# Kernel tuning notes

Hardware: AMD Instinct MI355X
Metric: run time of the kernel (lower is better)

## Reference

```python
import jax, jax.numpy as jnp
import numpy as np

EPS_T = 1e-4    # min ray t to count as a hit
BIG = 1e10      # sentinel for 'no hit'
NRM_EPS = 1e-12 # F.normalize eps


def _normalize(x):
    n = jnp.linalg.norm(x, axis=-1, keepdims=True)
    return x / jnp.maximum(n, NRM_EPS)


def _to_local(d, n):
    # Build orthonormal frame (s, t, n) from normal n (Duff et al. branchless),
    # then express d in that local frame: Frame.to_local.
    sign = jnp.where(n[..., 2] >= 0.0, 1.0, -1.0)
    a = -1.0 / (sign + n[..., 2])
    b = n[..., 0] * n[..., 1] * a
    s = jnp.stack([1.0 + sign * n[..., 0] ** 2 * a, sign * b, -sign * n[..., 0]], axis=-1)
    t = jnp.stack([b, sign + n[..., 1] ** 2 * a, -n[..., 1]], axis=-1)
    return jnp.stack([jnp.sum(d * s, -1), jnp.sum(d * t, -1), jnp.sum(d * n, -1)], axis=-1)


def setup_inputs() -> dict:
    key = jax.random.key(0)
    k = jax.random.split(key, 6)
    N, S, L = 524288, 128, 64
    ray_o = jax.random.normal(k[0], (N, 3), jnp.float32) * 5.0
    ray_d = jax.random.normal(k[1], (N, 3), jnp.float32)
    centers = jax.random.normal(k[2], (S, 3), jnp.float32) * 5.0
    radii = 0.5 + jax.random.uniform(k[3], (S,), jnp.float32)
    light_pos = jax.random.normal(k[4], (L, 3), jnp.float32) * 10.0
    light_idx = jax.random.randint(k[5], (N,), 0, L, jnp.int32)
    return {"ray_o": ray_o, "ray_d": ray_d, "centers": centers, "radii": radii,
            "light_pos": light_pos, "light_idx": light_idx}


def reference(ray_o, ray_d, centers, radii, light_pos, light_idx):
    # --- shapes.intersect(rays): brute-force nearest ray-sphere hit ---
    d = _normalize(ray_d)                                   # [N,3]
    od = jnp.sum(ray_o * d, -1)                             # [N]
    b = od[:, None] - jnp.einsum('nk,sk->ns', d, centers)   # [N,S]
    c = (jnp.sum(ray_o ** 2, -1)[:, None]
         - 2.0 * jnp.einsum('nk,sk->ns', ray_o, centers)
         + jnp.sum(centers ** 2, -1)[None, :]
         - radii[None, :] ** 2)                              # [N,S]
    disc = b * b - c
    t = -b - jnp.sqrt(jnp.maximum(disc, 0.0))
    valid = (disc > 0.0) & (t > EPS_T)
    t = jnp.where(valid, t, BIG)
    tmin = jnp.min(t, axis=1)                               # [N]
    sidx = jnp.argmin(t, axis=1)                            # [N]
    active = tmin < BIG                                     # [N] bool
    p = ray_o + tmin[:, None] * d                           # hit point [N,3]
    n = _normalize(p - centers[sidx])                       # surface normal [N,3]
    # --- sample_emitter_dir_wo_isect: direction to the sampled point light ---
    ds_d = light_pos[light_idx] - p                         # [N,3]
    # --- local-frame transform + normalize + where glue ---
    local = _to_local(ds_d, n)
    results = jnp.where(active[:, None], (_normalize(local) + 1.0) / 2.0,
                        jnp.zeros_like(ds_d))
    return (1.0 + results) / 2.0, active
```

## Files before the change

kernel.cpp:

```cpp
#include <hip/hip_runtime.h>
#include <math.h>

#define EPS_T 1e-4f
#define BIG 1e10f
#define NRM_EPS 1e-12f

#define PFB(R) \
  "ds_read_b128 " R ", %[lda]\n\t" \
  "v_add_u32 %[lda], 16, %[lda]\n\t"

#define SB(W, X, Y, Z, WN, GAP) \
  W \
  "v_mul_f32 v32, %[dz], " Z "\n\t" \
  "v_mul_f32 v33, %[oz], " Z "\n\t" \
  "v_fma_f32 v32, %[dy], " Y ", v32\n\t" \
  "v_fma_f32 v33, %[oy], " Y ", v33\n\t" \
  "v_fma_f32 v32, %[dx], " X ", v32\n\t" \
  "v_fma_f32 v33, %[ox], " X ", v33\n\t" \
  "v_add_f32 v34, v32, %[nod]\n\t" \
  "v_fma_f32 v35, v33, 2.0, %[noo]\n\t" \
  "v_add_f32 v35, v35, " WN "\n\t" \
  "v_fma_f32 v35, v34, v34, v35\n\t" \
  "v_sqrt_f32 v36, v35\n\t" \
  GAP \
  "v_sub_f32 v36, v34, v36\n\t" \
  "v_cmp_lt_f32 vcc, %[eps], v36\n\t" \
  "v_cmp_gt_f32 s[20:21], %[tmin], v36\n\t" \
  "s_and_b64 vcc, vcc, s[20:21]\n\t" \
  "v_cndmask_b32 %[tmin], %[tmin], v36, vcc\n\t" \
  "v_cndmask_b32 %[sidx], %[sidx], %[vj], vcc\n\t" \
  "v_add_u32 %[vj], 1, %[vj]\n\t"

#define W4 "s_waitcnt lgkmcnt(4)\n\t"

__global__ __launch_bounds__(256) void illum_kernel(
    const float* __restrict__ ray_o,
    const float* __restrict__ ray_d,
    const float* __restrict__ centers,
    const float* __restrict__ radii,
    const float* __restrict__ light_pos,
    const int*   __restrict__ light_idx,
    float* __restrict__ out,
    int N)
{
    __shared__ float4 tab[128];

    const int tid = threadIdx.x;
    if (tid < 128) {
        float cx = centers[3 * tid + 0];
        float cy = centers[3 * tid + 1];
        float cz = centers[3 * tid + 2];
        float r  = radii[tid];
        float w  = cx * cx + cy * cy + cz * cz - r * r;
        tab[tid] = make_float4(cx, cy, cz, -w);
    }
    __syncthreads();

    const int i = blockIdx.x * blockDim.x + tid;
    if (i >= N) return;

    float ox = ray_o[3 * i + 0], oy = ray_o[3 * i + 1], oz = ray_o[3 * i + 2];
    float dx = ray_d[3 * i + 0], dy = ray_d[3 * i + 1], dz = ray_d[3 * i + 2];

    float dn  = sqrtf(dx * dx + dy * dy + dz * dz);
    float din = 1.0f / fmaxf(dn, NRM_EPS);
    dx *= din; dy *= din; dz *= din;

    const float od = ox * dx + oy * dy + oz * dz;
    const float oo = ox * ox + oy * oy + oz * oz;
    const float nod = -od;
    const float noo = -oo;

    float tmin = BIG;
    int sidx = 0, vj = 0;
    unsigned lda = (unsigned)(size_t)&tab[0];

    asm volatile(
        "s_waitcnt lgkmcnt(0)\n\t"
        PFB("v[40:43]") PFB("v[44:47]") PFB("v[48:51]") PFB("v[52:55]") PFB("v[56:59]")
        ".rept 24\n\t"
        SB(W4, "v40","v41","v42","v43", PFB("v[40:43]"))
        SB(W4, "v44","v45","v46","v47", PFB("v[44:47]"))
        SB(W4, "v48","v49","v50","v51", PFB("v[48:51]"))
        SB(W4, "v52","v53","v54","v55", PFB("v[52:55]"))
        SB(W4, "v56","v57","v58","v59", PFB("v[56:59]"))
        ".endr\n\t"
        SB(W4, "v40","v41","v42","v43", PFB("v[40:43]"))
        SB(W4, "v44","v45","v46","v47", PFB("v[44:47]"))
        SB(W4, "v48","v49","v50","v51", PFB("v[48:51]"))
        SB("s_waitcnt lgkmcnt(4)\n\t", "v52","v53","v54","v55", "s_nop 1\n\t")
        SB("s_waitcnt lgkmcnt(3)\n\t", "v56","v57","v58","v59", "s_nop 1\n\t")
        SB("s_waitcnt lgkmcnt(2)\n\t", "v40","v41","v42","v43", "s_nop 1\n\t")
        SB("s_waitcnt lgkmcnt(1)\n\t", "v44","v45","v46","v47", "s_nop 1\n\t")
        SB("s_waitcnt lgkmcnt(0)\n\t", "v48","v49","v50","v51", "s_nop 1\n\t")
        : [tmin]"+v"(tmin), [sidx]"+v"(sidx), [vj]"+v"(vj), [lda]"+v"(lda)
        : [dx]"v"(dx), [dy]"v"(dy), [dz]"v"(dz),
          [ox]"v"(ox), [oy]"v"(oy), [oz]"v"(oz),
          [nod]"v"(nod), [noo]"v"(noo),
          [eps]"s"(1e-4f)
        : "v32","v33","v34","v35","v36",
          "v40","v41","v42","v43","v44","v45","v46","v47",
          "v48","v49","v50","v51","v52","v53","v54","v55",
          "v56","v57","v58","v59",
          "s20","s21","vcc","scc","memory");

    const bool active = (tmin < BIG);

    float px = fmaf(tmin, dx, ox);
    float py = fmaf(tmin, dy, oy);
    float pz = fmaf(tmin, dz, oz);

    float4 cb = tab[sidx];
    float nx = px - cb.x, ny = py - cb.y, nz = pz - cb.z;
    float nn  = sqrtf(nx * nx + ny * ny + nz * nz);
    float nin = 1.0f / fmaxf(nn, NRM_EPS);
    nx *= nin; ny *= nin; nz *= nin;

    int li = light_idx[i];
    float dsx = light_pos[3 * li + 0] - px;
    float dsy = light_pos[3 * li + 1] - py;
    float dsz = light_pos[3 * li + 2] - pz;

    float sgn = (nz >= 0.0f) ? 1.0f : -1.0f;
    float a   = -1.0f / (sgn + nz);
    float bb  = nx * ny * a;
    float sx = 1.0f + sgn * nx * nx * a, sy = sgn * bb,          sz = -sgn * nx;
    float tx = bb,                       ty = sgn + ny * ny * a, tz = -ny;

    float l0 = dsx * sx + dsy * sy + dsz * sz;
    float l1 = dsx * tx + dsy * ty + dsz * tz;
    float l2 = dsx * nx + dsy * ny + dsz * nz;
    float ln  = sqrtf(l0 * l0 + l1 * l1 + l2 * l2);
    float lin = 1.0f / fmaxf(ln, NRM_EPS);

    float r0 = active ? (l0 * lin + 1.0f) * 0.5f : 0.0f;
    float r1 = active ? (l1 * lin + 1.0f) * 0.5f : 0.0f;
    float r2 = active ? (l2 * lin + 1.0f) * 0.5f : 0.0f;

    out[3 * i + 0] = (1.0f + r0) * 0.5f;
    out[3 * i + 1] = (1.0f + r1) * 0.5f;
    out[3 * i + 2] = (1.0f + r2) * 0.5f;
    out[(size_t)3 * N + i] = active ? 1.0f : 0.0f;
}

extern "C" void kernel_launch(void* const* d_in, const int* in_sizes, int n_in,
                              void* d_out, int out_size, void* d_ws, size_t ws_size,
                              hipStream_t stream) {
    const float* ray_o     = (const float*)d_in[0];
    const float* ray_d     = (const float*)d_in[1];
    const float* centers   = (const float*)d_in[2];
    const float* radii     = (const float*)d_in[3];
    const float* light_pos = (const float*)d_in[4];
    const int*   light_idx = (const int*)d_in[5];
    float* out = (float*)d_out;

    const int N = in_sizes[0] / 3;

    const int block = 256;
    const int grid  = (N + block - 1) / block;
    illum_kernel<<<grid, block, 0, stream>>>(ray_o, ray_d, centers, radii,
                                             light_pos, light_idx, out, N);
}
```

Before: 34.88 us.

## Stream sphere table through scalar registers via s_load instead of LDS

Precomputes the sphere table (center, negated w) in a separate one-block prep kernel written to workspace. The main kernel drops the LDS table and its block barrier, and loads spheres with s_load_dwordx16 into SGPRs in double-buffered groups of four. Sphere operands then come from scalar registers shared across the wavefront, which removes per-lane ds_read traffic and VGPR pressure. The cost is a second kernel launch, a full lgkmcnt(0) wait per group that can stall the scalar pipeline, and reading the hit sphere's center from global memory afterwards.

```diff
diff --git a/kernel.cpp b/kernel.cpp
--- a/kernel.cpp
+++ b/kernel.cpp
@@ -5,24 +5,32 @@
 #define BIG 1e10f
 #define NRM_EPS 1e-12f
 
-#define PFB(R) \
-  "ds_read_b128 " R ", %[lda]\n\t" \
-  "v_add_u32 %[lda], 16, %[lda]\n\t"
+__global__ __launch_bounds__(128) void prep_kernel(
+    const float* __restrict__ centers, const float* __restrict__ radii,
+    float4* __restrict__ tb)
+{
+    int s = threadIdx.x;
+    float cx = centers[3 * s + 0];
+    float cy = centers[3 * s + 1];
+    float cz = centers[3 * s + 2];
+    float r  = radii[s];
+    float w  = cx * cx + cy * cy + cz * cz - r * r;
+    tb[s] = make_float4(cx, cy, cz, -w);
+}
 
-#define SB(W, X, Y, Z, WN, GAP) \
-  W \
-  "v_mul_f32 v32, %[dz], " Z "\n\t" \
-  "v_mul_f32 v33, %[oz], " Z "\n\t" \
-  "v_fma_f32 v32, %[dy], " Y ", v32\n\t" \
-  "v_fma_f32 v33, %[oy], " Y ", v33\n\t" \
-  "v_fma_f32 v32, %[dx], " X ", v32\n\t" \
-  "v_fma_f32 v33, %[ox], " X ", v33\n\t" \
+#define CS(CX, CY, CZ, NW) \
+  "v_mul_f32 v32, " CZ ", %[dz]\n\t" \
+  "v_mul_f32 v33, " CZ ", %[oz]\n\t" \
+  "v_fma_f32 v32, " CY ", %[dy], v32\n\t" \
+  "v_fma_f32 v33, " CY ", %[oy], v33\n\t" \
+  "v_fma_f32 v32, " CX ", %[dx], v32\n\t" \
+  "v_fma_f32 v33, " CX ", %[ox], v33\n\t" \
   "v_add_f32 v34, v32, %[nod]\n\t" \
   "v_fma_f32 v35, v33, 2.0, %[noo]\n\t" \
-  "v_add_f32 v35, v35, " WN "\n\t" \
+  "v_add_f32 v35, " NW ", v35\n\t" \
   "v_fma_f32 v35, v34, v34, v35\n\t" \
   "v_sqrt_f32 v36, v35\n\t" \
-  GAP \
+  "s_nop 1\n\t" \
   "v_sub_f32 v36, v34, v36\n\t" \
   "v_cmp_lt_f32 vcc, %[eps], v36\n\t" \
   "v_cmp_gt_f32 s[20:21], %[tmin], v36\n\t" \
@@ -31,32 +39,30 @@
   "v_cndmask_b32 %[sidx], %[sidx], %[vj], vcc\n\t" \
   "v_add_u32 %[vj], 1, %[vj]\n\t"
 
-#define W4 "s_waitcnt lgkmcnt(4)\n\t"
+#define CGA CS("s36","s37","s38","s39") CS("s40","s41","s42","s43") \
+            CS("s44","s45","s46","s47") CS("s48","s49","s50","s51")
+#define CGB CS("s52","s53","s54","s55") CS("s56","s57","s58","s59") \
+            CS("s60","s61","s62","s63") CS("s64","s65","s66","s67")
+
+#define LDA "s_load_dwordx16 s[36:51], s[30:31], 0x0\n\t" \
+            "s_add_u32 s30, s30, 64\n\t" \
+            "s_addc_u32 s31, s31, 0\n\t"
+#define LDB "s_load_dwordx16 s[52:67], s[30:31], 0x0\n\t" \
+            "s_add_u32 s30, s30, 64\n\t" \
+            "s_addc_u32 s31, s31, 0\n\t"
+#define WL  "s_waitcnt lgkmcnt(0)\n\t"
 
 __global__ __launch_bounds__(256) void illum_kernel(
     const float* __restrict__ ray_o,
     const float* __restrict__ ray_d,
     const float* __restrict__ centers,
-    const float* __restrict__ radii,
     const float* __restrict__ light_pos,
     const int*   __restrict__ light_idx,
+    const float* __restrict__ tb,
     float* __restrict__ out,
     int N)
 {
-    __shared__ float4 tab[128];
-
-    const int tid = threadIdx.x;
-    if (tid < 128) {
-        float cx = centers[3 * tid + 0];
-        float cy = centers[3 * tid + 1];
-        float cz = centers[3 * tid + 2];
-        float r  = radii[tid];
-        float w  = cx * cx + cy * cy + cz * cz - r * r;
-        tab[tid] = make_float4(cx, cy, cz, -w);
-    }
-    __syncthreads();
-
-    const int i = blockIdx.x * blockDim.x + tid;
+    const int i = blockIdx.x * blockDim.x + threadIdx.x;
     if (i >= N) return;
 
     float ox = ray_o[3 * i + 0], oy = ray_o[3 * i + 1], oz = ray_o[3 * i + 2];
@@ -73,36 +79,31 @@
 
     float tmin = BIG;
     int sidx = 0, vj = 0;
-    unsigned lda = (unsigned)(size_t)&tab[0];
 
     asm volatile(
-        "s_waitcnt lgkmcnt(0)\n\t"
-        PFB("v[40:43]") PFB("v[44:47]") PFB("v[48:51]") PFB("v[52:55]") PFB("v[56:59]")
-        ".rept 24\n\t"
-        SB(W4, "v40","v41","v42","v43", PFB("v[40:43]"))
-        SB(W4, "v44","v45","v46","v47", PFB("v[44:47]"))
-        SB(W4, "v48","v49","v50","v51", PFB("v[48:51]"))
-        SB(W4, "v52","v53","v54","v55", PFB("v[52:55]"))
-        SB(W4, "v56","v57","v58","v59", PFB("v[56:59]"))
+        "s_mov_b64 s[30:31], %[tb]\n\t"
+        WL
+        LDA
+        WL
+        ".rept 15\n\t"
+        LDB CGA WL
+        LDA CGB WL
         ".endr\n\t"
-        SB(W4, "v40","v41","v42","v43", PFB("v[40:43]"))
-        SB(W4, "v44","v45","v46","v47", PFB("v[44:47]"))
-        SB(W4, "v48","v49","v50","v51", PFB("v[48:51]"))
-        SB("s_waitcnt lgkmcnt(4)\n\t", "v52","v53","v54","v55", "s_nop 1\n\t")
-        SB("s_waitcnt lgkmcnt(3)\n\t", "v56","v57","v58","v59", "s_nop 1\n\t")
-        SB("s_waitcnt lgkmcnt(2)\n\t", "v40","v41","v42","v43", "s_nop 1\n\t")
-        SB("s_waitcnt lgkmcnt(1)\n\t", "v44","v45","v46","v47", "s_nop 1\n\t")
-        SB("s_waitcnt lgkmcnt(0)\n\t", "v48","v49","v50","v51", "s_nop 1\n\t")
-        : [tmin]"+v"(tmin), [sidx]"+v"(sidx), [vj]"+v"(vj), [lda]"+v"(lda)
+        LDB CGA WL
+        CGB
+        : [tmin]"+v"(tmin), [sidx]"+v"(sidx), [vj]"+v"(vj)
         : [dx]"v"(dx), [dy]"v"(dy), [dz]"v"(dz),
           [ox]"v"(ox), [oy]"v"(oy), [oz]"v"(oz),
           [nod]"v"(nod), [noo]"v"(noo),
-          [eps]"s"(1e-4f)
+          [eps]"s"(1e-4f),
+          [tb]"s"((unsigned long long)(size_t)tb)
         : "v32","v33","v34","v35","v36",
-          "v40","v41","v42","v43","v44","v45","v46","v47",
-          "v48","v49","v50","v51","v52","v53","v54","v55",
-          "v56","v57","v58","v59",
-          "s20","s21","vcc","scc","memory");
+          "s20","s21","s30","s31",
+          "s36","s37","s38","s39","s40","s41","s42","s43",
+          "s44","s45","s46","s47","s48","s49","s50","s51",
+          "s52","s53","s54","s55","s56","s57","s58","s59",
+          "s60","s61","s62","s63","s64","s65","s66","s67",
+          "vcc","scc","memory");
 
     const bool active = (tmin < BIG);
 
@@ -110,8 +111,10 @@
     float py = fmaf(tmin, dy, oy);
     float pz = fmaf(tmin, dz, oz);
 
-    float4 cb = tab[sidx];
-    float nx = px - cb.x, ny = py - cb.y, nz = pz - cb.z;
+    float cbx = centers[3 * sidx + 0];
+    float cby = centers[3 * sidx + 1];
+    float cbz = centers[3 * sidx + 2];
+    float nx = px - cbx, ny = py - cby, nz = pz - cbz;
     float nn  = sqrtf(nx * nx + ny * ny + nz * nz);
     float nin = 1.0f / fmaxf(nn, NRM_EPS);
     nx *= nin; ny *= nin; nz *= nin;
@@ -153,11 +156,15 @@
     const float* light_pos = (const float*)d_in[4];
     const int*   light_idx = (const int*)d_in[5];
     float* out = (float*)d_out;
+    float4* tb = (float4*)d_ws;
 
     const int N = in_sizes[0] / 3;
 
+    prep_kernel<<<1, 128, 0, stream>>>(centers, radii, tb);
+
     const int block = 256;
     const int grid  = (N + block - 1) / block;
-    illum_kernel<<<grid, block, 0, stream>>>(ray_o, ray_d, centers, radii,
-                                             light_pos, light_idx, out, N);
+    illum_kernel<<<grid, block, 0, stream>>>(ray_o, ray_d, centers,
+                                             light_pos, light_idx,
+                                             (const float*)tb, out, N);
 }
```

Result: slower. 39.19 us (+12.4%).
